# Kernel tuning notes

Hardware: AMD Instinct MI355X
Metric: run time of the kernel (lower is better)

Reference implementation:

```python
import math
import jax, jax.numpy as jnp
import numpy as np

B, N, T, H, DIN, NH = 4, 256, 30, 128, 3, 8
BN = B * N
DH = H // NH


def _pos_embed(t, h):
    pos = np.arange(t)[:, None].astype(np.float64)
    div = np.exp(np.arange(0, h, 2) * (-math.log(10000.0) / h))
    pe = np.zeros((t, h), np.float32)
    pe[:, 0::2] = np.sin(pos * div)
    pe[:, 1::2] = np.cos(pos * div)
    return jnp.asarray(pe)


def setup_inputs() -> dict:
    key = jax.random.key(0)
    ks = jax.random.split(key, 24)
    lin = lambda k, i, o: (jax.random.normal(k, (i, o), jnp.float32) / np.sqrt(i).astype(np.float32))
    vec = lambda k, o: jax.random.normal(k, (o,), jnp.float32) * 0.02
    return dict(
        x_raw=jax.random.normal(ks[0], (T, BN, DIN), jnp.float32),
        adjacency=jax.random.bernoulli(ks[1], 0.01, (T, BN, BN)).astype(jnp.float32),
        ego_mask=jax.random.bernoulli(ks[2], 0.5, (B, T, N)),
        W1=lin(ks[3], DIN, H), b1=vec(ks[4], H),
        W2=lin(ks[5], H, H), b2=vec(ks[6], H),
        Wq=lin(ks[7], H, H), bq=vec(ks[8], H),
        Wk=lin(ks[9], H, H), bk=vec(ks[10], H),
        Wv=lin(ks[11], H, H), bv=vec(ks[12], H),
        Wqi=lin(ks[13], H, H), bqi=vec(ks[14], H),
        Wki=lin(ks[15], H, H), bki=vec(ks[16], H),
        Wvi=lin(ks[17], H, H), bvi=vec(ks[18], H),
        Wo=lin(ks[19], H, H), bo=vec(ks[20], H),
    )


def reference(x_raw, adjacency, ego_mask,
              W1, b1, W2, b2,
              Wq, bq, Wk, bk, Wv, bv,
              Wqi, bqi, Wki, bki, Wvi, bvi,
              Wo, bo):
    # (B,T,N) -> (T, B*N) node-active mask, matching permute(1,0,2).reshape
    mask_flat = ego_mask.transpose(1, 0, 2).reshape(T, BN).astype(x_raw.dtype)

    def step(_, inp):
        x_t, A_t, m = inp  # (BN,DIN), (BN,BN), (BN,)
        # mask rows/cols (equiv. to gather A[idx][:,idx]) and add self loops
        A = A_t * m[:, None] * m[None, :] + jnp.diag(m)
        deg = A.sum(axis=1)
        dinv = jnp.where(deg > 0, 1.0, 0.0) * jax.lax.rsqrt(jnp.where(deg > 0, deg, 1.0))
        An = dinv[:, None] * A * dinv[None, :]  # D^-1/2 (A+I) D^-1/2
        h1 = jax.nn.relu(An @ (x_t @ W1) + b1)
        h2 = jax.nn.relu(An @ (h1 @ W2) + b2) * m[:, None]  # scatter back into zeros
        return None, h2

    _, hs = jax.lax.scan(step, None, (x_raw, adjacency, mask_flat))  # (T,BN,H)

    x_seq = hs.transpose(1, 0, 2) + _pos_embed(T, H)  # (BN,T,H)
    Q = x_seq @ Wq + bq
    K = x_seq @ Wk + bk
    V = x_seq @ Wv + bv
    # nn.MultiheadAttention applies its own in-projection to Q/K/V
    q = (Q @ Wqi + bqi).reshape(BN, T, NH, DH)
    k = (K @ Wki + bki).reshape(BN, T, NH, DH)
    v = (V @ Wvi + bvi).reshape(BN, T, NH, DH)
    attn = jax.nn.softmax(jnp.einsum('bthd,bshd->bhts', q, k) / np.sqrt(DH).astype(np.float32), axis=-1)
    o = jnp.einsum('bhts,bshd->bthd', attn, v).reshape(BN, T, H)
    out = (o @ Wo + bo).reshape(B, N, T, H)
    return out
```

## Files before the change

kernel.cpp:

```cpp
#include <hip/hip_runtime.h>
#include <hip/hip_bf16.h>
#include <math.h>

#define TT  30
#define BNN 1024
#define HH  128
#define MT  (TT*BNN)
#define CAP 64

typedef short bf16x8 __attribute__((ext_vector_type(8)));
typedef float f32x4 __attribute__((ext_vector_type(4)));

__device__ __forceinline__ float ldf(const void* p, size_t i, int fp) {
  if (fp == 0) {
    unsigned int w = ((unsigned int)(((const unsigned short*)p)[i])) << 16;
    float f; __builtin_memcpy(&f, &w, 4); return f;
  }
  return ((const float*)p)[i];
}
__device__ __forceinline__ float bf2f(unsigned short u) {
  unsigned int w = ((unsigned int)u) << 16;
  float f; __builtin_memcpy(&f, &w, 4); return f;
}
__device__ __forceinline__ unsigned short f2bf(float f) {
  unsigned int u; __builtin_memcpy(&u, &f, 4);
  return (unsigned short)((u + 0x7FFFu + ((u >> 16) & 1u)) >> 16);
}
__device__ __forceinline__ void splitbf(float a, unsigned short& h, unsigned short& l) {
  h = f2bf(a);
  l = f2bf(a - bf2f(h));
}

__global__ __launch_bounds__(1024) void detect_kernel(const unsigned char* xb, const unsigned char* eb, int* mode) {
  __shared__ int cnt_exp, f3F_odd1, f3F_any, fnz_notm4;
  int tid = threadIdx.x;
  if (tid == 0) { cnt_exp = 0; f3F_odd1 = 0; f3F_any = 0; fnz_notm4 = 0; }
  __syncthreads();
  int local = 0;
  for (int i = tid; i < 2048; i += 1024) {
    int e = (((const unsigned short*)xb)[i] >> 8) & 0x7F;
    if (e >= 0x3A && e <= 0x41) local++;
  }
  atomicAdd(&cnt_exp, local);
  int l1 = 0, l2 = 0, l3 = 0;
  for (int i = tid; i < 7680; i += 1024) {
    unsigned int w = ((const unsigned int*)eb)[i];
    #pragma unroll
    for (int e = 0; e < 4; ++e) {
      unsigned char b = (w >> (8 * e)) & 0xff;
      if (b == 0x3F) { l2 = 1; if (e == 1) l1 = 1; }
      if (b != 0 && e != 0) l3 = 1;
    }
  }
  if (l1) atomicOr(&f3F_odd1, 1);
  if (l2) atomicOr(&f3F_any, 1);
  if (l3) atomicOr(&fnz_notm4, 1);
  __syncthreads();
  if (tid == 0) {
    mode[0] = (cnt_exp > 1536) ? 0 : 1;
    mode[1] = f3F_odd1 ? 0 : (f3F_any ? 1 : (fnz_notm4 ? 2 : 3));
  }
}

__global__ __launch_bounds__(256) void setup_kernel(
    const void* ego,
    const void* W1, const void* b1, const void* W2, const void* b2, const void* Wo, const void* bo,
    const void* Wq, const void* bq, const void* Wk, const void* bk, const void* Wv, const void* bv,
    const void* Wqi, const void* bqi, const void* Wki, const void* bki, const void* Wvi, const void* bvi,
    const int* mode, float* pe, float* W1f, float* b1f, float* b2f, float* bof,
    unsigned short* W2h, unsigned short* W2l, unsigned short* Woh, unsigned short* Wol,
    unsigned short* Wch, unsigned short* Wcl, float* bqkv, float* maskf) {
  int bid = blockIdx.x;
  int fp = mode[0];
  if (bid < 15) {
    int idx = bid * 256 + threadIdx.x;
    if (idx >= TT * HH) return;
    int t = idx >> 7, i = idx & 127, j = i >> 1;
    double div = exp((double)(2 * j) * (-log(10000.0) / 128.0));
    double ang = (double)t * div;
    pe[idx] = (i & 1) ? (float)cos(ang) : (float)sin(ang);
    return;
  }
  if (bid < 146) {
    int idx = (bid - 15) * 256 + threadIdx.x;
    if (idx < 16384) { int k = idx >> 7, h = idx & 127; splitbf(ldf(W2, idx, fp), W2h[h * 128 + k], W2l[h * 128 + k]); return; }
    idx -= 16384;
    if (idx < 16384) { int k = idx >> 7, h = idx & 127; splitbf(ldf(Wo, idx, fp), Woh[h * 128 + k], Wol[h * 128 + k]); return; }
    idx -= 16384;
    if (idx < 384) { W1f[idx] = ldf(W1, idx, fp); return; } idx -= 384;
    if (idx < 128) { b1f[idx] = ldf(b1, idx, fp); return; } idx -= 128;
    if (idx < 128) { b2f[idx] = ldf(b2, idx, fp); return; } idx -= 128;
    if (idx < 128) { bof[idx] = ldf(bo, idx, fp); return; }
    return;
  }
  if (bid < 266) {
    int idx = (bid - 146) * 256 + threadIdx.x;
    if (idx >= MT) return;
    int t = idx >> 10, p = idx & 1023, b = p >> 8, n = p & 255;
    size_t e = (size_t)b * (TT * 256) + (size_t)t * 256 + n;
    int mm = mode[1];
    bool nz;
    if      (mm == 0) nz = ((const unsigned short*)ego)[e] != 0;
    else if (mm == 1) nz = ((const float*)ego)[e] != 0.f;
    else if (mm == 2) nz = ((const unsigned char*)ego)[e] != 0;
    else              nz = ((const int*)ego)[e] != 0;
    maskf[idx] = nz ? 1.f : 0.f;
    return;
  }
  int cb = bid - 266;
  int g = cb / 65;
  const void* Wa = (g == 0) ? Wq : (g == 1) ? Wk : Wv;
  const void* ba = (g == 0) ? bq : (g == 1) ? bk : bv;
  const void* Wb = (g == 0) ? Wqi : (g == 1) ? Wki : Wvi;
  const void* bb = (g == 0) ? bqi : (g == 1) ? bki : bvi;
  unsigned short* Wh = Wch + (size_t)g * 16384;
  unsigned short* Wl = Wcl + (size_t)g * 16384;
  float* bc = bqkv + g * 128;
  int idx = (cb % 65) * 256 + threadIdx.x;
  if (idx < 16384) {
    int k = idx >> 7, h = idx & 127;
    float s = 0.f;
    #pragma unroll 8
    for (int m = 0; m < 128; ++m) s += ldf(Wa, k * 128 + m, fp) * ldf(Wb, m * 128 + h, fp);
    splitbf(s, Wh[h * 128 + k], Wl[h * 128 + k]);
  } else if (idx < 16512) {
    int h = idx - 16384;
    float s = ldf(bb, h, fp);
    #pragma unroll 8
    for (int m = 0; m < 128; ++m) s += ldf(ba, m, fp) * ldf(Wb, m * 128 + h, fp);
    bc[h] = s;
  }
}

__global__ __launch_bounds__(256) void csr_kernel(const void* A, const int* mode, const float* maskf,
                                                  int* nnz, int* cols, float* dinv) {
  int fp = mode[0];
  int r = blockIdx.x * 4 + (threadIdx.x >> 6);
  int lane = threadIdx.x & 63;
  int t = r >> 10, i = r & 1023;
  int tb = t << 10;
  if (maskf[r] == 0.f) { if (lane == 0) { nnz[r] = 0; dinv[r] = 0.f; } return; }
  int* myc = cols + (size_t)r * CAP;
  int cnt = 0;
  unsigned long long lmask = (1ull << lane) - 1ull;
  if (fp == 1) {
    const float* Ar = (const float*)A + (size_t)t * BNN * BNN + (size_t)i * BNN;
    #pragma unroll
    for (int it = 0; it < 4; ++it) {
      int j0 = it * 256 + lane * 4;
      float4 av = *(const float4*)(Ar + j0);
      float4 mv = *(const float4*)(maskf + tb + j0);
      float va[4] = {av.x * mv.x, av.y * mv.y, av.z * mv.z, av.w * mv.w};
      #pragma unroll
      for (int e = 0; e < 4; ++e) {
        bool hit = va[e] != 0.f;
        unsigned long long bal = __ballot(hit);
        if (hit) { int pos = cnt + __popcll(bal & lmask); if (pos < CAP) myc[pos] = j0 + e; }
        cnt += __popcll(bal);
      }
    }
  } else {
    const unsigned short* Ar = (const unsigned short*)A + (size_t)t * BNN * BNN + (size_t)i * BNN;
    #pragma unroll
    for (int it = 0; it < 2; ++it) {
      int j0 = it * 512 + lane * 8;
      uint4 av = *(const uint4*)(Ar + j0);
      unsigned int wv[4] = {av.x, av.y, av.z, av.w};
      float4 m0 = *(const float4*)(maskf + tb + j0);
      float4 m1 = *(const float4*)(maskf + tb + j0 + 4);
      float mm[8] = {m0.x, m0.y, m0.z, m0.w, m1.x, m1.y, m1.z, m1.w};
      #pragma unroll
      for (int e = 0; e < 8; ++e) {
        unsigned short u = (wv[e >> 1] >> ((e & 1) * 16)) & 0xffff;
        bool hit = (u != 0) && (mm[e] != 0.f);
        unsigned long long bal = __ballot(hit);
        if (hit) { int pos = cnt + __popcll(bal & lmask); if (pos < CAP) myc[pos] = j0 + e; }
        cnt += __popcll(bal);
      }
    }
  }
  if (lane == 0) { nnz[r] = cnt > CAP ? CAP : cnt; dinv[r] = rsqrtf((float)cnt + 1.0f); }
}

__global__ __launch_bounds__(256) void spmm1_kernel(const void* x, const int* mode, const int* nnz,
    const int* cols, const float* dinv, const float* W1f, const float* b1f, float* h1) {
  int fp = mode[0];
  int r = blockIdx.x * 4 + (threadIdx.x >> 6);
  int lane = threadIdx.x & 63;
  int tbase = (r >> 10) << 10;
  int n = nnz[r];
  float s0 = 0.f, s1 = 0.f, s2 = 0.f;
  int j = -1;
  if (lane < n) j = tbase + cols[(size_t)r * CAP + lane];
  else if (lane == n) j = r;
  if (j >= 0) {
    float dj = dinv[j];
    s0 = dj * ldf(x, (size_t)j * 3 + 0, fp);
    s1 = dj * ldf(x, (size_t)j * 3 + 1, fp);
    s2 = dj * ldf(x, (size_t)j * 3 + 2, fp);
  }
  #pragma unroll
  for (int d = 1; d < 64; d <<= 1) {
    s0 += __shfl_xor(s0, d);
    s1 += __shfl_xor(s1, d);
    s2 += __shfl_xor(s2, d);
  }
  float dr = dinv[r];
  #pragma unroll
  for (int u = 0; u < 2; ++u) {
    int h = lane + u * 64;
    float v = dr * (s0 * W1f[h] + s1 * W1f[128 + h] + s2 * W1f[256 + h]) + b1f[h];
    h1[(size_t)r * 128 + h] = fmaxf(v, 0.f);
  }
}

__global__ __launch_bounds__(256) void spmm2_kernel(const float* g2s, const int* nnz, const int* cols,
    const float* dinv, const float* b2f, const float* maskf, const float* pe, float* xseq) {
  int r = blockIdx.x * 4 + (threadIdx.x >> 6);
  int lane = threadIdx.x & 63;
  int c = lane * 2;
  int t = r >> 10, i = r & 1023;
  int n = nnz[r];
  const int* myc = cols + (size_t)r * CAP;
  const float* st = g2s + ((size_t)(t << 10)) * 128;
  float2 acc = *(const float2*)(g2s + (size_t)r * 128 + c);
  for (int s = 0; s < n; ++s) {
    float2 v = *(const float2*)(st + (size_t)myc[s] * 128 + c);
    acc.x += v.x; acc.y += v.y;
  }
  float dr = dinv[r], m = maskf[r];
  float2 b = *(const float2*)(b2f + c);
  float2 p = *(const float2*)(pe + t * 128 + c);
  float vx = fmaxf(dr * acc.x + b.x, 0.f) * m + p.x;
  float vy = fmaxf(dr * acc.y + b.y, 0.f) * m + p.y;
  *(float2*)(xseq + ((size_t)i * TT + t) * 128 + c) = make_float2(vx, vy);
}

__global__ __launch_bounds__(256) void mfma_gemm(const float* A, const unsigned short* Bhi,
    const unsigned short* Blo, const float* scale, const float* bias,
    float* outf, void* outfin, const int* mode) {
  __shared__ __align__(16) unsigned short Ah[128 * 64];
  __shared__ __align__(16) unsigned short Al[128 * 64];
  __shared__ __align__(16) unsigned short Bh[128 * 64];
  __shared__ __align__(16) unsigned short Bl[128 * 64];
  int tid = threadIdx.x;
  int rowTile = blockIdx.x * 128;
  int gy = blockIdx.y;
  const unsigned short* Bhp = Bhi + (size_t)gy * 16384;
  const unsigned short* Blp = Blo + (size_t)gy * 16384;
  const float* bp = bias ? (bias + gy * 128) : nullptr;
  float* ofp = outf ? (outf + (size_t)gy * ((size_t)MT * 128)) : nullptr;

  int lane = tid & 63;
  int wid = tid >> 6;
  int wrow = (wid >> 1) * 64, wcol = (wid & 1) * 64;
  f32x4 acc[4][4];
  #pragma unroll
  for (int m = 0; m < 4; ++m)
    #pragma unroll
    for (int n = 0; n < 4; ++n) acc[m][n] = (f32x4){0.f, 0.f, 0.f, 0.f};

  for (int kb = 0; kb < 2; ++kb) {
    __syncthreads();
    #pragma unroll
    for (int it = 0; it < 4; ++it) {
      int c = it * 256 + tid;
      int r = c >> 3, cc = c & 7;
      int swz = (cc ^ (r & 7)) * 16;
      const float* ap = A + (size_t)(rowTile + r) * 128 + kb * 64 + cc * 8;
      float4 f0 = *(const float4*)ap;
      float4 f1 = *(const float4*)(ap + 4);
      float fa[8] = {f0.x, f0.y, f0.z, f0.w, f1.x, f1.y, f1.z, f1.w};
      unsigned short hi[8], lo[8];
      #pragma unroll
      for (int e = 0; e < 8; ++e) splitbf(fa[e], hi[e], lo[e]);
      uint4 ph, pl;
      ph.x = hi[0] | ((unsigned)hi[1] << 16); ph.y = hi[2] | ((unsigned)hi[3] << 16);
      ph.z = hi[4] | ((unsigned)hi[5] << 16); ph.w = hi[6] | ((unsigned)hi[7] << 16);
      pl.x = lo[0] | ((unsigned)lo[1] << 16); pl.y = lo[2] | ((unsigned)lo[3] << 16);
      pl.z = lo[4] | ((unsigned)lo[5] << 16); pl.w = lo[6] | ((unsigned)lo[7] << 16);
      *(uint4*)((char*)Ah + r * 128 + swz) = ph;
      *(uint4*)((char*)Al + r * 128 + swz) = pl;
      *(uint4*)((char*)Bh + r * 128 + swz) = *(const uint4*)(Bhp + (size_t)r * 128 + kb * 64 + cc * 8);
      *(uint4*)((char*)Bl + r * 128 + swz) = *(const uint4*)(Blp + (size_t)r * 128 + kb * 64 + cc * 8);
    }
    __syncthreads();
    #pragma unroll
    for (int ks = 0; ks < 2; ++ks) {
      bf16x8 ah[4], al[4], bh[4], bl[4];
      #pragma unroll
      for (int m = 0; m < 4; ++m) {
        int R = wrow + m * 16 + (lane & 15);
        int cc = ks * 4 + (lane >> 4);
        int off = R * 128 + ((cc ^ (R & 7)) * 16);
        ah[m] = *(const bf16x8*)((const char*)Ah + off);
        al[m] = *(const bf16x8*)((const char*)Al + off);
      }
      #pragma unroll
      for (int n = 0; n < 4; ++n) {
        int R = wcol + n * 16 + (lane & 15);
        int cc = ks * 4 + (lane >> 4);
        int off = R * 128 + ((cc ^ (R & 7)) * 16);
        bh[n] = *(const bf16x8*)((const char*)Bh + off);
        bl[n] = *(const bf16x8*)((const char*)Bl + off);
      }
      #pragma unroll
      for (int m = 0; m < 4; ++m)
        #pragma unroll
        for (int n = 0; n < 4; ++n) {
          acc[m][n] = __builtin_amdgcn_mfma_f32_16x16x32_bf16(ah[m], bl[n], acc[m][n], 0, 0, 0);
          acc[m][n] = __builtin_amdgcn_mfma_f32_16x16x32_bf16(al[m], bh[n], acc[m][n], 0, 0, 0);
          acc[m][n] = __builtin_amdgcn_mfma_f32_16x16x32_bf16(ah[m], bh[n], acc[m][n], 0, 0, 0);
        }
    }
  }
  int fp = mode[0];
  #pragma unroll
  for (int m = 0; m < 4; ++m) {
    #pragma unroll
    for (int n = 0; n < 4; ++n) {
      int col = wcol + n * 16 + (lane & 15);
      float bv = bp ? bp[col] : 0.f;
      #pragma unroll
      for (int q = 0; q < 4; ++q) {
        int row = rowTile + wrow + m * 16 + (lane >> 4) * 4 + q;
        float v = acc[m][n][q];
        if (scale) v *= scale[row];
        v += bv;
        size_t o = (size_t)row * 128 + col;
        if (ofp)           ofp[o] = v;
        else if (fp == 0)  ((unsigned short*)outfin)[o] = f2bf(v);
        else               ((float*)outfin)[o] = v;
      }
    }
  }
}

__global__ __launch_bounds__(256) void attn_kernel(const float* Q, const float* K, const float* V, float* O) {
  __shared__ __align__(16) float ksm[TT * 128];
  __shared__ __align__(16) float vsm[TT * 128];
  int tid = threadIdx.x;
  size_t base = (size_t)blockIdx.x * (TT * 128);
  for (int i = tid; i < TT * 128 / 4; i += 256) {
    ((float4*)ksm)[i] = ((const float4*)(K + base))[i];
    ((float4*)vsm)[i] = ((const float4*)(V + base))[i];
  }
  int h = tid >> 5, t = tid & 31;
  float q[16];
  if (t < TT) {
    const float4* qp = (const float4*)(Q + base + (size_t)t * 128 + h * 16);
    #pragma unroll
    for (int e = 0; e < 4; ++e) { float4 f = qp[e]; q[4*e] = f.x; q[4*e+1] = f.y; q[4*e+2] = f.z; q[4*e+3] = f.w; }
  }
  __syncthreads();
  if (t >= TT) return;
  float p[TT];
  float mx = -1e30f;
  #pragma unroll
  for (int s = 0; s < TT; ++s) {
    const float4* kp = (const float4*)&ksm[s * 128 + h * 16];
    float d = 0.f;
    #pragma unroll
    for (int e = 0; e < 4; ++e) {
      float4 f = kp[e];
      d += q[4*e] * f.x + q[4*e+1] * f.y + q[4*e+2] * f.z + q[4*e+3] * f.w;
    }
    p[s] = d * 0.25f;
    mx = fmaxf(mx, p[s]);
  }
  float sum = 0.f;
  #pragma unroll
  for (int s = 0; s < TT; ++s) { p[s] = __expf(p[s] - mx); sum += p[s]; }
  float inv = 1.f / sum;
  float o[16];
  #pragma unroll
  for (int e = 0; e < 16; ++e) o[e] = 0.f;
  #pragma unroll
  for (int s = 0; s < TT; ++s) {
    const float4* vp = (const float4*)&vsm[s * 128 + h * 16];
    float ps = p[s] * inv;
    #pragma unroll
    for (int e = 0; e < 4; ++e) {
      float4 f = vp[e];
      o[4*e] += ps * f.x; o[4*e+1] += ps * f.y; o[4*e+2] += ps * f.z; o[4*e+3] += ps * f.w;
    }
  }
  float* op = O + base + (size_t)t * 128 + h * 16;
  #pragma unroll
  for (int e = 0; e < 4; ++e)
    ((float4*)op)[e] = make_float4(o[4*e], o[4*e+1], o[4*e+2], o[4*e+3]);
}

extern "C" void kernel_launch(void* const* d_in, const int* in_sizes, int n_in,
                              void* d_out, int out_size, void* d_ws, size_t ws_size,
                              hipStream_t stream) {
  (void)in_sizes; (void)n_in; (void)out_size;
  const void* x_raw = d_in[0];
  const void* adj   = d_in[1];
  const void* ego   = d_in[2];
  const void* W1 = d_in[3];  const void* b1 = d_in[4];
  const void* W2 = d_in[5];  const void* b2 = d_in[6];
  const void* Wq = d_in[7];  const void* bq = d_in[8];
  const void* Wk = d_in[9];  const void* bk = d_in[10];
  const void* Wv = d_in[11]; const void* bv = d_in[12];
  const void* Wqi = d_in[13]; const void* bqi = d_in[14];
  const void* Wki = d_in[15]; const void* bki = d_in[16];
  const void* Wvi = d_in[17]; const void* bvi = d_in[18];
  const void* Wo = d_in[19]; const void* bo = d_in[20];

  char* w = (char*)d_ws;
  auto alloc = [&](size_t b) { char* p = w; w += (b + 255) & ~(size_t)255; return p; };
  int*   mode  = (int*)  alloc(16);
  float* maskf = (float*)alloc((size_t)MT * 4);
  float* dinv  = (float*)alloc((size_t)MT * 4);
  float* pe    = (float*)alloc((size_t)TT * HH * 4);
  float* W1f   = (float*)alloc(384 * 4);
  float* b1f   = (float*)alloc(128 * 4);
  float* b2f   = (float*)alloc(128 * 4);
  float* bof   = (float*)alloc(128 * 4);
  unsigned short* W2h = (unsigned short*)alloc(16384 * 2);
  unsigned short* W2l = (unsigned short*)alloc(16384 * 2);
  unsigned short* Woh = (unsigned short*)alloc(16384 * 2);
  unsigned short* Wol = (unsigned short*)alloc(16384 * 2);
  unsigned short* Wch = (unsigned short*)alloc((size_t)3 * 16384 * 2);
  unsigned short* Wcl = (unsigned short*)alloc((size_t)3 * 16384 * 2);
  float* bqkv  = (float*)alloc(3 * 128 * 4);
  int*   nnz   = (int*)  alloc((size_t)MT * 4);
  int*   cols  = (int*)  alloc((size_t)MT * CAP * 4);
  float* h1    = (float*)alloc((size_t)MT * 128 * 4);
  float* g2s   = (float*)alloc((size_t)MT * 128 * 4);
  float* xseq  = (float*)alloc((size_t)MT * 128 * 4);
  float* qkv   = (float*)alloc((size_t)3 * MT * 128 * 4);
  float* ob    = (float*)alloc((size_t)MT * 128 * 4);
  size_t need = (size_t)(w - (char*)d_ws);
  if (need > ws_size) return;

  detect_kernel<<<1, 1024, 0, stream>>>((const unsigned char*)x_raw, (const unsigned char*)ego, mode);
  setup_kernel<<<461, 256, 0, stream>>>(ego, W1, b1, W2, b2, Wo, bo,
                                        Wq, bq, Wk, bk, Wv, bv, Wqi, bqi, Wki, bki, Wvi, bvi,
                                        mode, pe, W1f, b1f, b2f, bof,
                                        W2h, W2l, Woh, Wol, Wch, Wcl, bqkv, maskf);
  csr_kernel<<<MT / 4, 256, 0, stream>>>(adj, mode, maskf, nnz, cols, dinv);
  spmm1_kernel<<<MT / 4, 256, 0, stream>>>(x_raw, mode, nnz, cols, dinv, W1f, b1f, h1);
  mfma_gemm<<<240, 256, 0, stream>>>(h1, W2h, W2l, dinv, nullptr, g2s, nullptr, mode);
  spmm2_kernel<<<MT / 4, 256, 0, stream>>>(g2s, nnz, cols, dinv, b2f, maskf, pe, xseq);
  mfma_gemm<<<dim3(240, 3), 256, 0, stream>>>(xseq, Wch, Wcl, nullptr, bqkv, qkv, nullptr, mode);
  attn_kernel<<<BNN, 256, 0, stream>>>(qkv, qkv + (size_t)MT * 128, qkv + (size_t)2 * MT * 128, ob);
  mfma_gemm<<<240, 256, 0, stream>>>(ob, Woh, Wol, nullptr, bof, nullptr, d_out, mode);
}
```

Measured before the change: 145.1 us.

## Fuse QKV projection, attention and output projection into one per-node kernel

Replaces the QKV GEMM, the attention kernel and the output GEMM with a single kernel per node sequence. Each block loads its 30x128 xseq tile into LDS as split-bf16, computes Q/K/V with MFMA into shared memory, runs attention, and applies the output projection in the same block. This removes the global round trips for qkv (3x) and the attention output, plus two kernel launches. The cost is higher LDS use per block (about 76KB), which limits occupancy, and weight fragments are re-read from global or L2 by every block.

```diff
diff --git a/kernel.cpp b/kernel.cpp
--- a/kernel.cpp
+++ b/kernel.cpp
@@ -336,59 +336,163 @@
   }
 }
 
-__global__ __launch_bounds__(256) void attn_kernel(const float* Q, const float* K, const float* V, float* O) {
-  __shared__ __align__(16) float ksm[TT * 128];
-  __shared__ __align__(16) float vsm[TT * 128];
-  int tid = threadIdx.x;
-  size_t base = (size_t)blockIdx.x * (TT * 128);
-  for (int i = tid; i < TT * 128 / 4; i += 256) {
-    ((float4*)ksm)[i] = ((const float4*)(K + base))[i];
-    ((float4*)vsm)[i] = ((const float4*)(V + base))[i];
-  }
+__global__ __launch_bounds__(256) void fused_tail_kernel(
+    const float* xseq,
+    const unsigned short* Wch, const unsigned short* Wcl, const float* bqkv,
+    const unsigned short* Woh, const unsigned short* Wol, const float* bof,
+    void* outfin, const int* mode) {
+  __shared__ __align__(16) unsigned short Ah[32 * 128];
+  __shared__ __align__(16) unsigned short Al[32 * 128];
+  __shared__ __align__(16) float qs[32 * 128];
+  __shared__ __align__(16) float ksm[32 * 128];
+  __shared__ __align__(16) float vsm[32 * 128];
+  int tid = threadIdx.x, lane = tid & 63, wid = tid >> 6;
+  int p = blockIdx.x;
+  const float* Ap = xseq + (size_t)p * (TT * 128);
+
+  for (int i = tid; i < 32 * 16; i += 256) {
+    int r = i >> 4, cc = i & 15;
+    int sw = (cc ^ (r & 7)) << 4;
+    uint4 ph = {0, 0, 0, 0}, pl = {0, 0, 0, 0};
+    if (r < TT) {
+      const float* ap = Ap + r * 128 + cc * 8;
+      float4 f0 = *(const float4*)ap, f1 = *(const float4*)(ap + 4);
+      float fa[8] = {f0.x, f0.y, f0.z, f0.w, f1.x, f1.y, f1.z, f1.w};
+      unsigned short hi[8], lo[8];
+      #pragma unroll
+      for (int e = 0; e < 8; ++e) splitbf(fa[e], hi[e], lo[e]);
+      ph.x = hi[0] | ((unsigned)hi[1] << 16); ph.y = hi[2] | ((unsigned)hi[3] << 16);
+      ph.z = hi[4] | ((unsigned)hi[5] << 16); ph.w = hi[6] | ((unsigned)hi[7] << 16);
+      pl.x = lo[0] | ((unsigned)lo[1] << 16); pl.y = lo[2] | ((unsigned)lo[3] << 16);
+      pl.z = lo[4] | ((unsigned)lo[5] << 16); pl.w = lo[6] | ((unsigned)lo[7] << 16);
+    }
+    *(uint4*)((char*)Ah + r * 256 + sw) = ph;
+    *(uint4*)((char*)Al + r * 256 + sw) = pl;
+  }
+  __syncthreads();
+
+  #pragma unroll
+  for (int j = 0; j < 12; ++j) {
+    int idx = wid * 12 + j;
+    int g = idx >> 4, rem = idx & 15, m = rem >> 3, n = rem & 7;
+    const unsigned short* Wh = Wch + (size_t)g * 16384;
+    const unsigned short* Wl = Wcl + (size_t)g * 16384;
+    f32x4 acc = (f32x4){0.f, 0.f, 0.f, 0.f};
+    int R = m * 16 + (lane & 15);
+    int rb = n * 16 + (lane & 15);
+    #pragma unroll
+    for (int ks = 0; ks < 4; ++ks) {
+      int cc = ks * 4 + (lane >> 4);
+      int offA = R * 256 + ((cc ^ (R & 7)) << 4);
+      bf16x8 ah = *(const bf16x8*)((const char*)Ah + offA);
+      bf16x8 al = *(const bf16x8*)((const char*)Al + offA);
+      bf16x8 bh = *(const bf16x8*)(Wh + (size_t)rb * 128 + cc * 8);
+      bf16x8 bl = *(const bf16x8*)(Wl + (size_t)rb * 128 + cc * 8);
+      acc = __builtin_amdgcn_mfma_f32_16x16x32_bf16(ah, bl, acc, 0, 0, 0);
+      acc = __builtin_amdgcn_mfma_f32_16x16x32_bf16(al, bh, acc, 0, 0, 0);
+      acc = __builtin_amdgcn_mfma_f32_16x16x32_bf16(ah, bh, acc, 0, 0, 0);
+    }
+    float* dst = (g == 0) ? qs : (g == 1) ? ksm : vsm;
+    int col = n * 16 + (lane & 15);
+    float bv = bqkv[g * 128 + col];
+    #pragma unroll
+    for (int q = 0; q < 4; ++q) {
+      int row = m * 16 + (lane >> 4) * 4 + q;
+      dst[row * 128 + col] = acc[q] + bv;
+    }
+  }
+  __syncthreads();
+
   int h = tid >> 5, t = tid & 31;
-  float q[16];
+  float o[16];
+  #pragma unroll
+  for (int e = 0; e < 16; ++e) o[e] = 0.f;
   if (t < TT) {
-    const float4* qp = (const float4*)(Q + base + (size_t)t * 128 + h * 16);
-    #pragma unroll
-    for (int e = 0; e < 4; ++e) { float4 f = qp[e]; q[4*e] = f.x; q[4*e+1] = f.y; q[4*e+2] = f.z; q[4*e+3] = f.w; }
+    float q[16];
+    #pragma unroll
+    for (int e = 0; e < 4; ++e) {
+      float4 f = ((const float4*)&qs[t * 128 + h * 16])[e];
+      q[4*e] = f.x; q[4*e+1] = f.y; q[4*e+2] = f.z; q[4*e+3] = f.w;
+    }
+    float pr[TT];
+    float mx = -1e30f;
+    #pragma unroll
+    for (int s = 0; s < TT; ++s) {
+      float d = 0.f;
+      #pragma unroll
+      for (int e = 0; e < 4; ++e) {
+        float4 f = ((const float4*)&ksm[s * 128 + h * 16])[e];
+        d += q[4*e] * f.x + q[4*e+1] * f.y + q[4*e+2] * f.z + q[4*e+3] * f.w;
+      }
+      pr[s] = d * 0.25f;
+      mx = fmaxf(mx, pr[s]);
+    }
+    float sum = 0.f;
+    #pragma unroll
+    for (int s = 0; s < TT; ++s) { pr[s] = __expf(pr[s] - mx); sum += pr[s]; }
+    float inv = 1.f / sum;
+    #pragma unroll
+    for (int s = 0; s < TT; ++s) {
+      float ps = pr[s] * inv;
+      #pragma unroll
+      for (int e = 0; e < 4; ++e) {
+        float4 f = ((const float4*)&vsm[s * 128 + h * 16])[e];
+        o[4*e] += ps * f.x; o[4*e+1] += ps * f.y; o[4*e+2] += ps * f.z; o[4*e+3] += ps * f.w;
+      }
+    }
+  }
+  #pragma unroll
+  for (int half = 0; half < 2; ++half) {
+    int cc = h * 2 + half;
+    int sw = (cc ^ (t & 7)) << 4;
+    uint4 ph = {0, 0, 0, 0}, pl = {0, 0, 0, 0};
+    if (t < TT) {
+      unsigned short hi[8], lo[8];
+      #pragma unroll
+      for (int e = 0; e < 8; ++e) splitbf(o[half * 8 + e], hi[e], lo[e]);
+      ph.x = hi[0] | ((unsigned)hi[1] << 16); ph.y = hi[2] | ((unsigned)hi[3] << 16);
+      ph.z = hi[4] | ((unsigned)hi[5] << 16); ph.w = hi[6] | ((unsigned)hi[7] << 16);
+      pl.x = lo[0] | ((unsigned)lo[1] << 16); pl.y = lo[2] | ((unsigned)lo[3] << 16);
+      pl.z = lo[4] | ((unsigned)lo[5] << 16); pl.w = lo[6] | ((unsigned)lo[7] << 16);
+    }
+    *(uint4*)((char*)Ah + t * 256 + sw) = ph;
+    *(uint4*)((char*)Al + t * 256 + sw) = pl;
   }
   __syncthreads();
-  if (t >= TT) return;
-  float p[TT];
-  float mx = -1e30f;
-  #pragma unroll
-  for (int s = 0; s < TT; ++s) {
-    const float4* kp = (const float4*)&ksm[s * 128 + h * 16];
-    float d = 0.f;
-    #pragma unroll
-    for (int e = 0; e < 4; ++e) {
-      float4 f = kp[e];
-      d += q[4*e] * f.x + q[4*e+1] * f.y + q[4*e+2] * f.z + q[4*e+3] * f.w;
-    }
-    p[s] = d * 0.25f;
-    mx = fmaxf(mx, p[s]);
-  }
-  float sum = 0.f;
-  #pragma unroll
-  for (int s = 0; s < TT; ++s) { p[s] = __expf(p[s] - mx); sum += p[s]; }
-  float inv = 1.f / sum;
-  float o[16];
-  #pragma unroll
-  for (int e = 0; e < 16; ++e) o[e] = 0.f;
-  #pragma unroll
-  for (int s = 0; s < TT; ++s) {
-    const float4* vp = (const float4*)&vsm[s * 128 + h * 16];
-    float ps = p[s] * inv;
-    #pragma unroll
-    for (int e = 0; e < 4; ++e) {
-      float4 f = vp[e];
-      o[4*e] += ps * f.x; o[4*e+1] += ps * f.y; o[4*e+2] += ps * f.z; o[4*e+3] += ps * f.w;
-    }
-  }
-  float* op = O + base + (size_t)t * 128 + h * 16;
-  #pragma unroll
-  for (int e = 0; e < 4; ++e)
-    ((float4*)op)[e] = make_float4(o[4*e], o[4*e+1], o[4*e+2], o[4*e+3]);
+
+  int fp = mode[0];
+  #pragma unroll
+  for (int j = 0; j < 4; ++j) {
+    int idx = wid * 4 + j;
+    int m = idx >> 3, n = idx & 7;
+    f32x4 acc = (f32x4){0.f, 0.f, 0.f, 0.f};
+    int R = m * 16 + (lane & 15);
+    int rb = n * 16 + (lane & 15);
+    #pragma unroll
+    for (int ks = 0; ks < 4; ++ks) {
+      int cc = ks * 4 + (lane >> 4);
+      int offA = R * 256 + ((cc ^ (R & 7)) << 4);
+      bf16x8 ah = *(const bf16x8*)((const char*)Ah + offA);
+      bf16x8 al = *(const bf16x8*)((const char*)Al + offA);
+      bf16x8 bh = *(const bf16x8*)(Woh + (size_t)rb * 128 + cc * 8);
+      bf16x8 bl = *(const bf16x8*)(Wol + (size_t)rb * 128 + cc * 8);
+      acc = __builtin_amdgcn_mfma_f32_16x16x32_bf16(ah, bl, acc, 0, 0, 0);
+      acc = __builtin_amdgcn_mfma_f32_16x16x32_bf16(al, bh, acc, 0, 0, 0);
+      acc = __builtin_amdgcn_mfma_f32_16x16x32_bf16(ah, bh, acc, 0, 0, 0);
+    }
+    int col = n * 16 + (lane & 15);
+    float bv = bof[col];
+    #pragma unroll
+    for (int q = 0; q < 4; ++q) {
+      int row = m * 16 + (lane >> 4) * 4 + q;
+      if (row < TT) {
+        float v = acc[q] + bv;
+        size_t oidx = ((size_t)p * TT + row) * 128 + col;
+        if (fp == 0) ((unsigned short*)outfin)[oidx] = f2bf(v);
+        else         ((float*)outfin)[oidx] = v;
+      }
+    }
+  }
 }
 
 extern "C" void kernel_launch(void* const* d_in, const int* in_sizes, int n_in,
@@ -430,8 +534,6 @@
   float* h1    = (float*)alloc((size_t)MT * 128 * 4);
   float* g2s   = (float*)alloc((size_t)MT * 128 * 4);
   float* xseq  = (float*)alloc((size_t)MT * 128 * 4);
-  float* qkv   = (float*)alloc((size_t)3 * MT * 128 * 4);
-  float* ob    = (float*)alloc((size_t)MT * 128 * 4);
   size_t need = (size_t)(w - (char*)d_ws);
   if (need > ws_size) return;
 
@@ -444,7 +546,5 @@
   spmm1_kernel<<<MT / 4, 256, 0, stream>>>(x_raw, mode, nnz, cols, dinv, W1f, b1f, h1);
   mfma_gemm<<<240, 256, 0, stream>>>(h1, W2h, W2l, dinv, nullptr, g2s, nullptr, mode);
   spmm2_kernel<<<MT / 4, 256, 0, stream>>>(g2s, nnz, cols, dinv, b2f, maskf, pe, xseq);
-  mfma_gemm<<<dim3(240, 3), 256, 0, stream>>>(xseq, Wch, Wcl, nullptr, bqkv, qkv, nullptr, mode);
-  attn_kernel<<<BNN, 256, 0, stream>>>(qkv, qkv + (size_t)MT * 128, qkv + (size_t)2 * MT * 128, ob);
-  mfma_gemm<<<240, 256, 0, stream>>>(ob, Woh, Wol, nullptr, bof, nullptr, d_out, mode);
-}
+  fused_tail_kernel<<<BNN, 256, 0, stream>>>(xseq, Wch, Wcl, bqkv, Woh, Wol, bof, d_out, mode);
+}
```

Result: slower. 160.8 us (+10.9%).
